# Kernel optimization log

Hardware: AMD Instinct MI355X
Metric: run time of the kernel (lower is better)

## Reference

```python
import jax, jax.numpy as jnp
import numpy as np

B, H, W, C = 2, 256, 256, 192
HEADS, WS, SHIFT = 6, 8, 4
N = WS * WS              # tokens per window = 64
NW = (H // WS) * (W // WS)  # windows per image = 1024
DH = C // HEADS
HID = 4 * C
EPS = 1e-5


def _rel_pos_index(ws):
    coords = np.stack(np.meshgrid(np.arange(ws), np.arange(ws), indexing='ij'))  # (2, ws, ws)
    flat = coords.reshape(2, -1)
    rel = flat[:, :, None] - flat[:, None, :]           # (2, N, N)
    rel = rel.transpose(1, 2, 0).astype(np.int64)       # (N, N, 2)
    rel[:, :, 0] += ws - 1
    rel[:, :, 1] += ws - 1
    rel[:, :, 0] *= 2 * ws - 1
    return rel.sum(-1).astype(np.int32)                 # (N, N)


def _attn_mask(h, w, ws, shift):
    img = np.zeros((h, w), np.float32)
    slc = (slice(0, -ws), slice(-ws, -shift), slice(-shift, None))
    cnt = 0
    for hs in slc:
        for wcol in slc:
            img[hs, wcol] = cnt
            cnt += 1
    mw = img.reshape(h // ws, ws, w // ws, ws).transpose(0, 2, 1, 3).reshape(-1, ws * ws)
    am = mw[:, None, :] - mw[:, :, None]
    return np.where(am != 0, np.float32(-100.0), np.float32(0.0)).astype(np.float32)


def setup_inputs() -> dict:
    key = jax.random.key(0)
    ks = jax.random.split(key, 8)
    s = 0.02
    return {
        'x': jax.random.normal(ks[0], (B, H * W, C), jnp.float32),
        'ln1_g': jnp.ones((C,), jnp.float32),
        'ln1_b': jnp.zeros((C,), jnp.float32),
        'qkv_w': jax.random.normal(ks[1], (3 * C, C), jnp.float32) * s,
        'qkv_b': jnp.zeros((3 * C,), jnp.float32),
        'rpb_table': jax.random.normal(ks[2], ((2 * WS - 1) ** 2, HEADS), jnp.float32) * s,
        'proj_w': jax.random.normal(ks[3], (C, C), jnp.float32) * s,
        'proj_b': jnp.zeros((C,), jnp.float32),
        'ln2_g': jnp.ones((C,), jnp.float32),
        'ln2_b': jnp.zeros((C,), jnp.float32),
        'fc1_w': jax.random.normal(ks[4], (HID, C), jnp.float32) * s,
        'fc1_b': jnp.zeros((HID,), jnp.float32),
        'fc2_w': jax.random.normal(ks[5], (C, HID), jnp.float32) * s,
        'fc2_b': jnp.zeros((C,), jnp.float32),
        'attn_mask': jnp.asarray(_attn_mask(H, W, WS, SHIFT)),   # (NW, N, N)
        'rel_idx': jnp.asarray(_rel_pos_index(WS)),               # (N, N) int32
    }


def _ln(x, g, b):
    m = jnp.mean(x, axis=-1, keepdims=True)
    v = jnp.mean(jnp.square(x - m), axis=-1, keepdims=True)
    return (x - m) * jax.lax.rsqrt(v + EPS) * g + b


def reference(x, ln1_g, ln1_b, qkv_w, qkv_b, rpb_table, proj_w, proj_b,
              ln2_g, ln2_b, fc1_w, fc1_b, fc2_w, fc2_b, attn_mask, rel_idx):
    nH, nW = H // WS, W // WS
    shortcut = x
    h = _ln(x, ln1_g, ln1_b).reshape(B, H, W, C)
    # cyclic shift
    h = jnp.roll(h, (-SHIFT, -SHIFT), axis=(1, 2))
    # window partition -> (B*NW, N, C)
    wins = h.reshape(B, nH, WS, nW, WS, C).transpose(0, 1, 3, 2, 4, 5).reshape(B * NW, N, C)
    qkv = wins @ qkv_w.T + qkv_b                       # (B*NW, N, 3C)
    qkv = qkv.reshape(B * NW, N, 3, HEADS, DH).transpose(2, 0, 3, 1, 4)
    q, k, v = qkv[0], qkv[1], qkv[2]                   # (B*NW, heads, N, DH)
    scale = DH ** -0.5
    attn = jnp.einsum('bhnd,bhmd->bhnm', q * scale, k)  # (B*NW, heads, N, N)
    bias = rpb_table[rel_idx.reshape(-1)].reshape(N, N, HEADS).transpose(2, 0, 1)
    attn = attn + bias[None]
    # shifted-window mask: per-window additive mask
    attn = attn.reshape(B, NW, HEADS, N, N) + attn_mask[None, :, None]
    attn = jax.nn.softmax(attn, axis=-1).reshape(B * NW, HEADS, N, N)
    out = jnp.einsum('bhnm,bhmd->bhnd', attn, v)        # (B*NW, heads, N, DH)
    out = out.transpose(0, 2, 1, 3).reshape(B * NW, N, C)
    out = out @ proj_w.T + proj_b
    # window reverse + unshift
    out = out.reshape(B, nH, nW, WS, WS, C).transpose(0, 1, 3, 2, 4, 5).reshape(B, H, W, C)
    out = jnp.roll(out, (SHIFT, SHIFT), axis=(1, 2)).reshape(B, H * W, C)
    x = shortcut + out
    h2 = _ln(x, ln2_g, ln2_b)
    h2 = jax.nn.gelu(h2 @ fc1_w.T + fc1_b, approximate=False)
    return x + (h2 @ fc2_w.T + fc2_b)
```

## Files before the change

### kernel.cpp

```cpp
#include <hip/hip_runtime.h>
#include <hip/hip_bf16.h>
#include <math.h>

using bf16 = __hip_bfloat16;
typedef short bfrag __attribute__((ext_vector_type(8)));
typedef float f32x4 __attribute__((ext_vector_type(4)));

__device__ __forceinline__ float b2f(bf16 v){ return __bfloat162float(v); }
__device__ __forceinline__ bf16  f2b(float v){ return __float2bfloat16(v); }
__device__ __forceinline__ short f2bs(float v){ bf16 t = f2b(v); union{bf16 h; short s;} u; u.h = t; return u.s; }
__device__ __forceinline__ float bits2f(unsigned short s){ union{unsigned u; float f;} c; c.u = ((unsigned)s) << 16; return c.f; }
__device__ __forceinline__ int   pk2(float lo, float hi){
  return (((int)(unsigned short)f2bs(hi)) << 16) | (int)(unsigned short)f2bs(lo);
}
__device__ __forceinline__ float ldT(const float* p, long long i){ return p[i]; }
__device__ __forceinline__ float ldT(const bf16*  p, long long i){ return __bfloat162float(p[i]); }

__device__ __forceinline__ bfrag ldfrag(const bf16* p){ return *reinterpret_cast<const bfrag*>(p); }
__device__ __forceinline__ f32x4 mm16(bfrag a, bfrag b, f32x4 c){
  return __builtin_amdgcn_mfma_f32_16x16x32_bf16(a, b, c, 0, 0, 0);
}

template<int CTRL>
__device__ __forceinline__ float dppf(float v){
  union{float f; int i;} u; u.f = v;
  u.i = __builtin_amdgcn_update_dpp(0, u.i, CTRL, 0xF, 0xF, true);
  return u.f;
}
__device__ __forceinline__ float rmax16(float v){
  v = fmaxf(v, dppf<0xB1>(v));  v = fmaxf(v, dppf<0x4E>(v));
  v = fmaxf(v, dppf<0x141>(v)); v = fmaxf(v, dppf<0x140>(v));
  return v;
}
__device__ __forceinline__ float rsum16(float v){
  v += dppf<0xB1>(v);  v += dppf<0x4E>(v);
  v += dppf<0x141>(v); v += dppf<0x140>(v);
  return v;
}
__device__ __forceinline__ float rsum4(float v){
  v += dppf<0xB1>(v); v += dppf<0x4E>(v);
  return v;
}

__device__ __forceinline__ int reg1(int g){ return (g >= 248) + (g >= 252); }
__device__ __forceinline__ long long natidx(int gw, int t){
  const int wl = gw & 1023;
  const int sr = (((wl >> 5) << 3) + (t >> 3) + 4) & 255;
  const int sc = (((wl & 31) << 3) + (t & 7) + 4) & 255;
  return (((long long)(gw >> 10)) << 16) + sr*256 + sc;
}

template<typename T>
__device__ __forceinline__ void ld48(const T* p, long long off, float* d){
  if constexpr (sizeof(T) == 4){
    #pragma unroll
    for (int i = 0; i < 12; ++i){
      float4 v = *reinterpret_cast<const float4*>((const float*)p + off + i*4);
      d[i*4+0]=v.x; d[i*4+1]=v.y; d[i*4+2]=v.z; d[i*4+3]=v.w;
    }
  } else {
    #pragma unroll
    for (int i = 0; i < 6; ++i){
      bfrag v = *reinterpret_cast<const bfrag*>((const bf16*)p + off + i*8);
      #pragma unroll
      for (int j = 0; j < 8; ++j) d[i*8+j] = bits2f((unsigned short)v[j]);
    }
  }
}

#define WS_QKV   0
#define WS_PROJ  221184
#define WS_FC1   294912
#define WS_FC2   589824
#define WS_BIAS6 884736

__global__ __launch_bounds__(256) void prep_k(const void* det,
    const void* qkvw, const void* projw, const void* fc1w, const void* fc2w,
    const void* rpb, const int* __restrict__ relidx, char* wsb)
{
  const bool isbf = (((const unsigned short*)det)[0] == 0x3F80u);
  const int gt = blockIdx.x * 256 + threadIdx.x;
  if (gt < 55296) {
    const int fid = gt >> 6, l = gt & 63;
    int f, nkt, ckw; const void* src; bf16* dst;
    if (fid < 216)      { f = fid;       nkt = 6;  ckw = 192; src = qkvw;  dst = (bf16*)(wsb + WS_QKV); }
    else if (fid < 288) { f = fid - 216; nkt = 6;  ckw = 192; src = projw; dst = (bf16*)(wsb + WS_PROJ); }
    else if (fid < 576) { f = fid - 288; nkt = 6;  ckw = 192; src = fc1w;  dst = (bf16*)(wsb + WS_FC1); }
    else                { f = fid - 576; nkt = 24; ckw = 768; src = fc2w;  dst = (bf16*)(wsb + WS_FC2); }
    const int ct = f / nkt, kt = f - ct * nkt;
    const long long ro = (long long)(ct*16 + (l & 15)) * ckw + kt*32 + (l >> 4)*8;
    bf16* dp = dst + ((long long)f * 64 + l) * 8;
    #pragma unroll
    for (int j = 0; j < 8; ++j) {
      float v = isbf ? b2f(((const bf16*)src)[ro + j]) : ((const float*)src)[ro + j];
      dp[j] = f2b(v);
    }
  } else if (gt < 55296 + 24576) {
    const int t = gt - 55296;
    const int h = t >> 12, ij = t & 4095;
    const int ri = relidx[ij];
    float v = isbf ? b2f(((const bf16*)rpb)[ri*6 + h]) : ((const float*)rpb)[ri*6 + h];
    ((float*)(wsb + WS_BIAS6))[t] = v;
  }
}

#define XN_S 200
#define QK_S 72
#define VT_S 72
#define LDS_K1 (64*XN_S*2 + 64*QK_S*2 + 32*VT_S*2)

template<typename T>
__device__ void attn_body(const T* __restrict__ x, const T* __restrict__ g1, const T* __restrict__ b1,
                          const bf16* __restrict__ qkvwp, const T* __restrict__ qkvb,
                          const bf16* __restrict__ projwp, const T* __restrict__ projb,
                          const float* __restrict__ bias6, char* __restrict__ dout,
                          int x2f32, char* smem)
{
  bf16* xn = (bf16*)smem;
  bf16* qk = xn + 64*XN_S;
  bf16* vt = qk + 64*QK_S;
  const int tid = threadIdx.x, l = tid & 63, w = tid >> 6;
  const int lr = l & 15, lg = l >> 4;
  const int gw = blockIdx.x;
  const int wl = gw & 1023, wi = wl >> 5, wj = wl & 31;

  {
    const int t = (w << 4) + (l >> 2);
    const int c0 = (l & 3) * 48;
    const long long base = natidx(gw, t) * 192 + c0;
    float xv[48];
    ld48(x, base, xv);
    float s1 = 0.f, s2 = 0.f;
    #pragma unroll
    for (int i = 0; i < 48; ++i){ s1 += xv[i]; s2 = fmaf(xv[i], xv[i], s2); }
    s1 = rsum4(s1); s2 = rsum4(s2);
    const float m  = s1 * (1.f/192.f);
    const float rs = rsqrtf(s2*(1.f/192.f) - m*m + 1e-5f);
    bf16* xr = xn + t*XN_S + c0;
    #pragma unroll
    for (int cb = 0; cb < 6; ++cb){
      bfrag o;
      #pragma unroll
      for (int j = 0; j < 8; ++j){
        const int c = cb*8 + j;
        o[j] = f2bs((xv[c]-m)*rs*ldT(g1, c0+c) + ldT(b1, c0+c));
      }
      *reinterpret_cast<bfrag*>(xr + cb*8) = o;
    }
  }
  __syncthreads();

  int rjh[4], rjw[4], rih[4], riw[4];
  #pragma unroll
  for (int ct = 0; ct < 4; ++ct){
    const int j = ct*16 + lr;
    rjh[ct] = reg1(wi*8 + (j >> 3));
    rjw[ct] = reg1(wj*8 + (j & 7));
  }
  #pragma unroll
  for (int r = 0; r < 4; ++r){
    const int i = w*16 + lg*4 + r;
    rih[r] = reg1(wi*8 + (i >> 3));
    riw[r] = reg1(wj*8 + (i & 7));
  }

  int ohpk[6][2][2];

  #pragma unroll
  for (int h = 0; h < 6; ++h){
    f32x4 acc[6];
    #pragma unroll
    for (int u = 0; u < 6; ++u) acc[u] = (f32x4){0.f,0.f,0.f,0.f};
    #pragma unroll
    for (int kt = 0; kt < 6; ++kt){
      bfrag a = ldfrag(&xn[(w*16 + lr)*XN_S + kt*32 + lg*8]);
      bfrag bq[6];
      #pragma unroll
      for (int u = 0; u < 6; ++u){
        const int ctg = (u >> 1)*12 + 2*h + (u & 1);
        bq[u] = ldfrag(qkvwp + ((long long)(ctg*6 + kt)*64 + l)*8);
      }
      #pragma unroll
      for (int u = 0; u < 6; ++u) acc[u] = mm16(a, bq[u], acc[u]);
    }
    __syncthreads();

    #pragma unroll
    for (int u = 0; u < 6; ++u){
      const int ctg = (u >> 1)*12 + 2*h + (u & 1);
      const float bia = ldT(qkvb, ctg*16 + lr);
      #pragma unroll
      for (int r = 0; r < 4; ++r){
        const int row = w*16 + lg*4 + r;
        const float v = acc[u][r] + bia;
        if (u < 2)      qk[row*QK_S + u*16 + lr] = f2b(v * 0.17677669529663687f);
        else if (u < 4) qk[row*QK_S + 32 + (u & 1)*16 + lr] = f2b(v);
        else            vt[((u & 1)*16 + lr)*VT_S + row] = f2b(v);
      }
    }
    __syncthreads();

    f32x4 s4[4];
    {
      bfrag aq = ldfrag(&qk[(w*16 + lr)*QK_S + lg*8]);
      #pragma unroll
      for (int ct = 0; ct < 4; ++ct)
        s4[ct] = mm16(aq, ldfrag(&qk[(ct*16 + lr)*QK_S + 32 + lg*8]), (f32x4){0.f,0.f,0.f,0.f});
    }
    const float* bh = bias6 + h*4096;
    float pr[4][4], inv4[4];
    #pragma unroll
    for (int r = 0; r < 4; ++r){
      const int i = w*16 + lg*4 + r;
      const int ib = i*64 + lr;
      float v[4];
      #pragma unroll
      for (int ct = 0; ct < 4; ++ct){
        const float msk = (rih[r] == rjh[ct] && riw[r] == rjw[ct]) ? 0.f : -100.f;
        v[ct] = s4[ct][r] + bh[ib + ct*16] + msk;
      }
      float mx = rmax16(fmaxf(fmaxf(v[0],v[1]), fmaxf(v[2],v[3])));
      v[0] = __expf(v[0]-mx); v[1] = __expf(v[1]-mx);
      v[2] = __expf(v[2]-mx); v[3] = __expf(v[3]-mx);
      const float sm = rsum16(v[0]+v[1]+v[2]+v[3]);
      inv4[r] = __fdividef(1.f, sm);
      pr[r][0]=v[0]; pr[r][1]=v[1]; pr[r][2]=v[2]; pr[r][3]=v[3];
    }
    __syncthreads();

    #pragma unroll
    for (int r = 0; r < 4; ++r){
      const int i = w*16 + lg*4 + r;
      #pragma unroll
      for (int ct = 0; ct < 4; ++ct)
        qk[i*QK_S + ct*16 + lr] = f2b(pr[r][ct]*inv4[r]);
    }
    f32x4 o2[2] = {(f32x4){0.f,0.f,0.f,0.f}, (f32x4){0.f,0.f,0.f,0.f}};
    #pragma unroll
    for (int ktp = 0; ktp < 2; ++ktp){
      bfrag ap = ldfrag(&qk[(w*16 + lr)*QK_S + ktp*32 + lg*8]);
      o2[0] = mm16(ap, ldfrag(&vt[(lr)*VT_S + ktp*32 + lg*8]), o2[0]);
      o2[1] = mm16(ap, ldfrag(&vt[(16 + lr)*VT_S + ktp*32 + lg*8]), o2[1]);
    }
    #pragma unroll
    for (int u = 0; u < 2; ++u){
      ohpk[h][u][0] = pk2(o2[u][0], o2[u][1]);
      ohpk[h][u][1] = pk2(o2[u][2], o2[u][3]);
    }
  }

  #pragma unroll
  for (int h = 0; h < 6; ++h)
    #pragma unroll
    for (int u = 0; u < 2; ++u)
      #pragma unroll
      for (int rr = 0; rr < 2; ++rr){
        const int pk = ohpk[h][u][rr];
        const int row = w*16 + lg*4 + rr*2;
        *reinterpret_cast<short*>(&xn[row*XN_S + h*32 + u*16 + lr]) = (short)(pk & 0xffff);
        *reinterpret_cast<short*>(&xn[(row+1)*XN_S + h*32 + u*16 + lr]) = (short)(((unsigned)pk) >> 16);
      }
  __syncthreads();

  const int mp = w >> 1, chh = w & 1;
  f32x4 pacc[2][6];
  #pragma unroll
  for (int mt = 0; mt < 2; ++mt)
    #pragma unroll
    for (int cc = 0; cc < 6; ++cc) pacc[mt][cc] = (f32x4){0.f,0.f,0.f,0.f};
  #pragma unroll
  for (int kt = 0; kt < 6; ++kt){
    bfrag a0 = ldfrag(&xn[(mp*32 + lr)*XN_S + kt*32 + lg*8]);
    bfrag a1 = ldfrag(&xn[(mp*32 + 16 + lr)*XN_S + kt*32 + lg*8]);
    #pragma unroll
    for (int cc = 0; cc < 6; ++cc){
      bfrag bp = ldfrag(projwp + ((long long)((chh*6 + cc)*6 + kt)*64 + l)*8);
      pacc[0][cc] = mm16(a0, bp, pacc[0][cc]);
      pacc[1][cc] = mm16(a1, bp, pacc[1][cc]);
    }
  }
  #pragma unroll
  for (int mt = 0; mt < 2; ++mt)
    #pragma unroll
    for (int r = 0; r < 4; ++r){
      const int t = mp*32 + mt*16 + lg*4 + r;
      const long long n = natidx(gw, t);
      #pragma unroll
      for (int cc = 0; cc < 6; ++cc){
        const int c = (chh*6 + cc)*16 + lr;
        const float y = pacc[mt][cc][r] + ldT(projb, c) + ldT(x, n*192 + c);
        if (x2f32) ((float*)(dout + n*768))[c] = y;
        else       ((bf16*)(dout + n*384))[c]  = f2b(y);
      }
    }
}

__global__ __launch_bounds__(256, 4) void swin_attn_k(
    const void* det, const void* x, const void* g1, const void* b1,
    const bf16* qkvwp, const void* qkvb, const bf16* projwp, const void* projb,
    const float* bias6, void* doutv)
{
  extern __shared__ char smem[];
  const bool isbf = (((const unsigned short*)det)[0] == 0x3F80u);
  char* dout = (char*)doutv;
  if (isbf)
    attn_body<bf16>((const bf16*)x, (const bf16*)g1, (const bf16*)b1, qkvwp,
                    (const bf16*)qkvb, projwp, (const bf16*)projb, bias6, dout, 0, smem);
  else
    attn_body<float>((const float*)x, (const float*)g1, (const float*)b1, qkvwp,
                     (const float*)qkvb, projwp, (const float*)projb, bias6, dout, 1, smem);
}

#define HS_S 72
#define LDS_K3 (48*512*2 + 128*HS_S*2)

template<typename T>
__device__ void mlp_body(const T* __restrict__ g2, const T* __restrict__ b2,
                         const bf16* __restrict__ fc1p, const T* __restrict__ fb1,
                         const bf16* __restrict__ fc2p, const T* __restrict__ fb2,
                         char* __restrict__ dout, int outf32, char* smem)
{
  bf16* xn2 = (bf16*)smem;
  bf16* bw  = (bf16*)smem;
  bf16* hs  = bw + 48*512;
  const int tid = threadIdx.x, l = tid & 63, w = tid >> 6;
  const int lr = l & 15, lg = l >> 4;
  const long long t0 = (long long)blockIdx.x * 128;

  #pragma unroll
  for (int it = 0; it < 2; ++it){
    const int t = w*32 + it*16 + (l >> 2);
    const int c0 = (l & 3) * 48;
    const long long n = t0 + t;
    float xv[48];
    if (outf32) ld48((const float*)(dout + n*768), c0, xv);
    else        ld48((const bf16*)(dout + n*384), c0, xv);
    float s1 = 0.f, s2 = 0.f;
    #pragma unroll
    for (int i = 0; i < 48; ++i){ s1 += xv[i]; s2 = fmaf(xv[i], xv[i], s2); }
    s1 = rsum4(s1); s2 = rsum4(s2);
    const float m  = s1 * (1.f/192.f);
    const float rs = rsqrtf(s2*(1.f/192.f) - m*m + 1e-5f);
    bf16* xr = xn2 + t*XN_S + c0;
    #pragma unroll
    for (int cb = 0; cb < 6; ++cb){
      bfrag o;
      #pragma unroll
      for (int j = 0; j < 8; ++j){
        const int c = cb*8 + j;
        o[j] = f2bs((xv[c]-m)*rs*ldT(g2, c0+c) + ldT(b2, c0+c));
      }
      *reinterpret_cast<bfrag*>(xr + cb*8) = o;
    }
  }
  __syncthreads();

  bfrag xa[2][6];
  #pragma unroll
  for (int mt = 0; mt < 2; ++mt)
    #pragma unroll
    for (int kt = 0; kt < 6; ++kt)
      xa[mt][kt] = ldfrag(&xn2[(w*32 + mt*16 + lr)*XN_S + kt*32 + lg*8]);
  __syncthreads();

  f32x4 fa[2][12];
  #pragma unroll
  for (int mt = 0; mt < 2; ++mt)
    #pragma unroll
    for (int ct = 0; ct < 12; ++ct) fa[mt][ct] = (f32x4){0.f,0.f,0.f,0.f};

  for (int c = 0; c < 12; ++c){
    {
      const int q0 = w*12;
      #pragma unroll
      for (int gg = 0; gg < 4; ++gg){
        bfrag tmp[3];
        #pragma unroll
        for (int e = 0; e < 3; ++e){
          const int q = q0 + gg*3 + e;
          const bf16* src = (q < 24)
            ? fc1p + ((long long)(c*24 + q)*64 + l)*8
            : fc2p + ((long long)(((q-24) >> 1)*24 + c*2 + ((q-24) & 1))*64 + l)*8;
          tmp[e] = ldfrag(src);
        }
        #pragma unroll
        for (int e = 0; e < 3; ++e){
          const int q = q0 + gg*3 + e;
          *reinterpret_cast<bfrag*>(bw + (q*64 + l)*8) = tmp[e];
        }
      }
    }
    __syncthreads();
    f32x4 a1[2][4];
    #pragma unroll
    for (int mt = 0; mt < 2; ++mt)
      #pragma unroll
      for (int u = 0; u < 4; ++u) a1[mt][u] = (f32x4){0.f,0.f,0.f,0.f};
    #pragma unroll
    for (int kt = 0; kt < 6; ++kt)
      #pragma unroll
      for (int u = 0; u < 4; ++u){
        bfrag bq = ldfrag(&bw[((u*6 + kt)*64 + l)*8]);
        a1[0][u] = mm16(xa[0][kt], bq, a1[0][u]);
        a1[1][u] = mm16(xa[1][kt], bq, a1[1][u]);
      }
    #pragma unroll
    for (int u = 0; u < 4; ++u){
      const float bia = ldT(fb1, c*64 + u*16 + lr);
      #pragma unroll
      for (int mt = 0; mt < 2; ++mt)
        #pragma unroll
        for (int r = 0; r < 4; ++r){
          const float xv = a1[mt][u][r] + bia;
          const float g  = __fdividef(xv, 1.f + __expf(-1.702f*xv));
          hs[(w*32 + mt*16 + lg*4 + r)*HS_S + u*16 + lr] = f2b(g);
        }
    }
    #pragma unroll
    for (int ktl = 0; ktl < 2; ++ktl){
      bfrag aH0 = ldfrag(&hs[(w*32 + lr)*HS_S + ktl*32 + lg*8]);
      bfrag aH1 = ldfrag(&hs[(w*32 + 16 + lr)*HS_S + ktl*32 + lg*8]);
      #pragma unroll
      for (int ct = 0; ct < 12; ++ct){
        bfrag bq = ldfrag(&bw[((24 + ct*2 + ktl)*64 + l)*8]);
        fa[0][ct] = mm16(aH0, bq, fa[0][ct]);
        fa[1][ct] = mm16(aH1, bq, fa[1][ct]);
      }
    }
    __syncthreads();
  }

  #pragma unroll
  for (int mt = 0; mt < 2; ++mt)
    #pragma unroll
    for (int r = 0; r < 4; ++r){
      const long long n = t0 + w*32 + mt*16 + lg*4 + r;
      #pragma unroll
      for (int ct = 0; ct < 12; ++ct){
        const int cc = ct*16 + lr;
        float resid = outf32 ? ((const float*)(dout + n*768))[cc]
                             : b2f(((const bf16*)(dout + n*384))[cc]);
        const float y = fa[mt][ct][r] + ldT(fb2, cc) + resid;
        if (outf32) ((float*)(dout + n*768))[cc] = y;
        else        ((bf16*)(dout + n*384))[cc]  = f2b(y);
      }
    }
}

__global__ __launch_bounds__(256, 2) void swin_mlp_k(
    const void* det, const void* g2, const void* b2, const bf16* fc1p, const void* fb1,
    const bf16* fc2p, const void* fb2, void* doutv)
{
  extern __shared__ char smem[];
  const bool isbf = (((const unsigned short*)det)[0] == 0x3F80u);
  char* dout = (char*)doutv;
  if (isbf)
    mlp_body<bf16>((const bf16*)g2, (const bf16*)b2, fc1p, (const bf16*)fb1,
                   fc2p, (const bf16*)fb2, dout, 0, smem);
  else
    mlp_body<float>((const float*)g2, (const float*)b2, fc1p, (const float*)fb1,
                    fc2p, (const float*)fb2, dout, 1, smem);
}

extern "C" void kernel_launch(void* const* d_in, const int* in_sizes, int n_in,
                              void* d_out, int out_size, void* d_ws, size_t ws_size,
                              hipStream_t stream)
{
  (void)in_sizes; (void)n_in; (void)out_size; (void)ws_size;
  char* ws = (char*)d_ws;

  (void)hipFuncSetAttribute((const void*)swin_attn_k, hipFuncAttributeMaxDynamicSharedMemorySize, LDS_K1);
  (void)hipFuncSetAttribute((const void*)swin_mlp_k,  hipFuncAttributeMaxDynamicSharedMemorySize, LDS_K3);

  prep_k<<<dim3(312), dim3(256), 0, stream>>>(
      d_in[1], d_in[3], d_in[6], d_in[10], d_in[12], d_in[5], (const int*)d_in[15], ws);

  swin_attn_k<<<dim3(2048), dim3(256), LDS_K1, stream>>>(
      d_in[1], d_in[0], d_in[1], d_in[2],
      (const bf16*)(ws + WS_QKV), d_in[4], (const bf16*)(ws + WS_PROJ), d_in[7],
      (const float*)(ws + WS_BIAS6), d_out);

  swin_mlp_k<<<dim3(1024), dim3(256), LDS_K3, stream>>>(
      d_in[1], d_in[8], d_in[9],
      (const bf16*)(ws + WS_FC1), d_in[11], (const bf16*)(ws + WS_FC2), d_in[13], d_out);
}
```

Baseline: 332.9 us.

## Store intermediate residual in bf16 workspace and batch MLP weight staging loads

The post-attention residual x2 was kept in fp32 in the output buffer. It now goes to a separate bf16 workspace buffer when the workspace is large enough, which halves the bytes written by the attention kernel and read back twice by the MLP kernel. The MLP weight staging loop now issues all 12 fragment loads before any LDS stores, giving more loads in flight at the cost of more registers. Rounding x2 to bf16 adds precision loss on the residual path.

```diff
diff --git a/kernel.cpp b/kernel.cpp
--- a/kernel.cpp
+++ b/kernel.cpp
@@ -73,6 +73,8 @@
 #define WS_FC1   294912
 #define WS_FC2   589824
 #define WS_BIAS6 884736
+#define WS_X2    1048576
+#define X2BF_BYTES ((size_t)131072 * 192 * 2)
 
 __global__ __launch_bounds__(256) void prep_k(const void* det,
     const void* qkvw, const void* projw, const void* fc1w, const void* fc2w,
@@ -113,8 +115,8 @@
 __device__ void attn_body(const T* __restrict__ x, const T* __restrict__ g1, const T* __restrict__ b1,
                           const bf16* __restrict__ qkvwp, const T* __restrict__ qkvb,
                           const bf16* __restrict__ projwp, const T* __restrict__ projb,
-                          const float* __restrict__ bias6, char* __restrict__ dout,
-                          int x2f32, char* smem)
+                          const float* __restrict__ bias6, char* __restrict__ x2p,
+                          int x2bf, char* smem)
 {
   bf16* xn = (bf16*)smem;
   bf16* qk = xn + 64*XN_S;
@@ -289,8 +291,8 @@
       for (int cc = 0; cc < 6; ++cc){
         const int c = (chh*6 + cc)*16 + lr;
         const float y = pacc[mt][cc][r] + ldT(projb, c) + ldT(x, n*192 + c);
-        if (x2f32) ((float*)(dout + n*768))[c] = y;
-        else       ((bf16*)(dout + n*384))[c]  = f2b(y);
+        if (x2bf) ((bf16*)(x2p + n*384))[c]  = f2b(y);
+        else      ((float*)(x2p + n*768))[c] = y;
       }
     }
 }
@@ -298,17 +300,17 @@
 __global__ __launch_bounds__(256, 4) void swin_attn_k(
     const void* det, const void* x, const void* g1, const void* b1,
     const bf16* qkvwp, const void* qkvb, const bf16* projwp, const void* projb,
-    const float* bias6, void* doutv)
+    const float* bias6, void* x2pv, int x2bf)
 {
   extern __shared__ char smem[];
   const bool isbf = (((const unsigned short*)det)[0] == 0x3F80u);
-  char* dout = (char*)doutv;
+  char* x2p = (char*)x2pv;
   if (isbf)
     attn_body<bf16>((const bf16*)x, (const bf16*)g1, (const bf16*)b1, qkvwp,
-                    (const bf16*)qkvb, projwp, (const bf16*)projb, bias6, dout, 0, smem);
+                    (const bf16*)qkvb, projwp, (const bf16*)projb, bias6, x2p, 1, smem);
   else
     attn_body<float>((const float*)x, (const float*)g1, (const float*)b1, qkvwp,
-                     (const float*)qkvb, projwp, (const float*)projb, bias6, dout, 1, smem);
+                     (const float*)qkvb, projwp, (const float*)projb, bias6, x2p, x2bf, smem);
 }
 
 #define HS_S 72
@@ -318,6 +320,7 @@
 __device__ void mlp_body(const T* __restrict__ g2, const T* __restrict__ b2,
                          const bf16* __restrict__ fc1p, const T* __restrict__ fb1,
                          const bf16* __restrict__ fc2p, const T* __restrict__ fb2,
+                         const char* __restrict__ x2p, int x2bf,
                          char* __restrict__ dout, int outf32, char* smem)
 {
   bf16* xn2 = (bf16*)smem;
@@ -333,8 +336,8 @@
     const int c0 = (l & 3) * 48;
     const long long n = t0 + t;
     float xv[48];
-    if (outf32) ld48((const float*)(dout + n*768), c0, xv);
-    else        ld48((const bf16*)(dout + n*384), c0, xv);
+    if (x2bf) ld48((const bf16*)(x2p + n*384), c0, xv);
+    else      ld48((const float*)(x2p + n*768), c0, xv);
     float s1 = 0.f, s2 = 0.f;
     #pragma unroll
     for (int i = 0; i < 48; ++i){ s1 += xv[i]; s2 = fmaf(xv[i], xv[i], s2); }
@@ -372,23 +375,18 @@
   for (int c = 0; c < 12; ++c){
     {
       const int q0 = w*12;
-      #pragma unroll
-      for (int gg = 0; gg < 4; ++gg){
-        bfrag tmp[3];
-        #pragma unroll
-        for (int e = 0; e < 3; ++e){
-          const int q = q0 + gg*3 + e;
-          const bf16* src = (q < 24)
-            ? fc1p + ((long long)(c*24 + q)*64 + l)*8
-            : fc2p + ((long long)(((q-24) >> 1)*24 + c*2 + ((q-24) & 1))*64 + l)*8;
-          tmp[e] = ldfrag(src);
-        }
-        #pragma unroll
-        for (int e = 0; e < 3; ++e){
-          const int q = q0 + gg*3 + e;
-          *reinterpret_cast<bfrag*>(bw + (q*64 + l)*8) = tmp[e];
-        }
-      }
+      bfrag tmp[12];
+      #pragma unroll
+      for (int e = 0; e < 12; ++e){
+        const int q = q0 + e;
+        const bf16* src = (q < 24)
+          ? fc1p + ((long long)(c*24 + q)*64 + l)*8
+          : fc2p + ((long long)(((q-24) >> 1)*24 + c*2 + ((q-24) & 1))*64 + l)*8;
+        tmp[e] = ldfrag(src);
+      }
+      #pragma unroll
+      for (int e = 0; e < 12; ++e)
+        *reinterpret_cast<bfrag*>(bw + ((q0 + e)*64 + l)*8) = tmp[e];
     }
     __syncthreads();
     f32x4 a1[2][4];
@@ -438,8 +436,8 @@
       #pragma unroll
       for (int ct = 0; ct < 12; ++ct){
         const int cc = ct*16 + lr;
-        float resid = outf32 ? ((const float*)(dout + n*768))[cc]
-                             : b2f(((const bf16*)(dout + n*384))[cc]);
+        float resid = x2bf ? b2f(((const bf16*)(x2p + n*384))[cc])
+                           : ((const float*)(x2p + n*768))[cc];
         const float y = fa[mt][ct][r] + ldT(fb2, cc) + resid;
         if (outf32) ((float*)(dout + n*768))[cc] = y;
         else        ((bf16*)(dout + n*384))[cc]  = f2b(y);
@@ -449,25 +447,30 @@
 
 __global__ __launch_bounds__(256, 2) void swin_mlp_k(
     const void* det, const void* g2, const void* b2, const bf16* fc1p, const void* fb1,
-    const bf16* fc2p, const void* fb2, void* doutv)
+    const bf16* fc2p, const void* fb2, const void* x2pv, int x2bf, void* doutv)
 {
   extern __shared__ char smem[];
   const bool isbf = (((const unsigned short*)det)[0] == 0x3F80u);
   char* dout = (char*)doutv;
+  const char* x2p = (const char*)x2pv;
   if (isbf)
     mlp_body<bf16>((const bf16*)g2, (const bf16*)b2, fc1p, (const bf16*)fb1,
-                   fc2p, (const bf16*)fb2, dout, 0, smem);
+                   fc2p, (const bf16*)fb2, x2p, 1, dout, 0, smem);
   else
     mlp_body<float>((const float*)g2, (const float*)b2, fc1p, (const float*)fb1,
-                    fc2p, (const float*)fb2, dout, 1, smem);
+                    fc2p, (const float*)fb2, x2p, x2bf, dout, 1, smem);
 }
 
 extern "C" void kernel_launch(void* const* d_in, const int* in_sizes, int n_in,
                               void* d_out, int out_size, void* d_ws, size_t ws_size,
                               hipStream_t stream)
 {
-  (void)in_sizes; (void)n_in; (void)out_size; (void)ws_size;
+  (void)in_sizes; (void)n_in; (void)out_size;
   char* ws = (char*)d_ws;
+
+  const int ws_ok = (ws_size >= (size_t)WS_X2 + X2BF_BYTES) ? 1 : 0;
+  void* x2p = ws_ok ? (void*)(ws + WS_X2) : d_out;
+  const int x2bf = ws_ok ? 1 : 0;
 
   (void)hipFuncSetAttribute((const void*)swin_attn_k, hipFuncAttributeMaxDynamicSharedMemorySize, LDS_K1);
   (void)hipFuncSetAttribute((const void*)swin_mlp_k,  hipFuncAttributeMaxDynamicSharedMemorySize, LDS_K3);
@@ -478,9 +481,10 @@
   swin_attn_k<<<dim3(2048), dim3(256), LDS_K1, stream>>>(
       d_in[1], d_in[0], d_in[1], d_in[2],
       (const bf16*)(ws + WS_QKV), d_in[4], (const bf16*)(ws + WS_PROJ), d_in[7],
-      (const float*)(ws + WS_BIAS6), d_out);
+      (const float*)(ws + WS_BIAS6), x2p, x2bf);
 
   swin_mlp_k<<<dim3(1024), dim3(256), LDS_K3, stream>>>(
       d_in[1], d_in[8], d_in[9],
-      (const bf16*)(ws + WS_FC1), d_in[11], (const bf16*)(ws + WS_FC2), d_in[13], d_out);
-}
+      (const bf16*)(ws + WS_FC1), d_in[11], (const bf16*)(ws + WS_FC2), d_in[13],
+      x2p, x2bf, d_out);
+}
```

Result: slower. 352.8 us (+6.0%).
